# Kernel optimization log

Hardware: AMD Instinct MI355X
Metric: run time of the kernel (lower is better)

Reference implementation:

```python
import jax, jax.numpy as jnp
import numpy as np

H = 2048
V = 32000
N = 2048  # batch*seq tokens
IGNORE_INDEX = -100
TEMPERATURE = 1.0
W_HARD = 0.5
W_SOFT = 0.5


def setup_inputs() -> dict:
    key = jax.random.key(0)
    k1, k2, k3, k4, k5 = jax.random.split(key, 5)
    student_input = jax.random.normal(k1, (N, H // 2), dtype=jnp.float32)
    teacher_input = jax.random.normal(k2, (N, H), dtype=jnp.float32)
    target = jax.random.randint(k3, (N,), 0, V, dtype=jnp.int64)
    # learned params: Linear(in, out=V, bias=False) -> weight shape (V, in)
    student_weight = jax.random.normal(k4, (V, H // 2), dtype=jnp.float32) * 0.02
    teacher_weight = jax.random.normal(k5, (V, H), dtype=jnp.float32) * 0.02
    return {
        "student_input": student_input,
        "teacher_input": teacher_input,
        "student_weight": student_weight,
        "teacher_weight": teacher_weight,
        "target": target,
    }


def reference(student_input, teacher_input, student_weight, teacher_weight, target):
    # Linear projections to vocab (teacher under no_grad in torch)
    student_logits = (student_input @ student_weight.T).astype(jnp.float32)  # (N, V)
    teacher_logits = jax.lax.stop_gradient(
        (teacher_input @ teacher_weight.T).astype(jnp.float32)
    )  # (N, V)

    # Hard loss: cross-entropy with ignore_index, mean over valid tokens
    log_probs = jax.nn.log_softmax(student_logits, axis=-1)
    valid = target != IGNORE_INDEX
    safe_tgt = jnp.where(valid, target, 0)
    nll = -jnp.take_along_axis(log_probs, safe_tgt[:, None], axis=-1)[:, 0]
    n_valid = jnp.maximum(valid.sum(), 1)
    hard_loss = jnp.sum(jnp.where(valid, nll, 0.0)) / n_valid

    # Soft loss: Jensen-Shannon divergence with batchmean reduction
    sl = student_logits / TEMPERATURE
    tl = teacher_logits / TEMPERATURE
    student_probs = jax.nn.softmax(sl, axis=-1)
    teacher_probs = jax.nn.softmax(tl, axis=-1)
    log_mean = jnp.log((student_probs + teacher_probs) * 0.5)
    log_sp = jnp.log(student_probs)
    log_tp = jnp.log(teacher_probs)
    n = sl.shape[0]
    # kl_div(log_mean, log_p, log_target=True, batchmean) = sum(p*(log_p - log_mean))/n
    student_kl = jnp.sum(student_probs * (log_sp - log_mean)) / n
    teacher_kl = jnp.sum(teacher_probs * (log_tp - log_mean)) / n
    jsd_loss = (student_kl + teacher_kl) * 0.5

    return W_HARD * hard_loss + W_SOFT * jsd_loss
```

## Files before the change

kernel.cpp:

```cpp
#include <hip/hip_runtime.h>

#define VOCAB 32000
#define NTOK 2048
#define IGNORE_INDEX (-100)

typedef unsigned short u16;
typedef unsigned int u32;
typedef __bf16 bf16x8 __attribute__((ext_vector_type(8)));
typedef float floatx4 __attribute__((ext_vector_type(4)));

__device__ __forceinline__ u16 f2bf(float f) {
    u32 u = __float_as_uint(f);
    u32 r = u + 0x7fffu + ((u >> 16) & 1u);
    return (u16)(r >> 16);
}
__device__ __forceinline__ float bf2f(u32 lo16) {
    return __uint_as_float(lo16 << 16);
}

__global__ __launch_bounds__(256) void cvt_kernel(const float* __restrict__ in,
                                                  u16* __restrict__ out, int n4) {
    int i = blockIdx.x * 256 + threadIdx.x;
    if (i >= n4) return;
    float4 v = ((const float4*)in)[i];
    ushort4 o;
    o.x = f2bf(v.x); o.y = f2bf(v.y); o.z = f2bf(v.z); o.w = f2bf(v.w);
    ((ushort4*)out)[i] = o;
}

__global__ __launch_bounds__(256) void gemm_bt_kernel(
    const u16* __restrict__ A, const u16* __restrict__ B, u16* __restrict__ C,
    int M, int N, int K)
{
    __shared__ u16 lds_a[128 * 64];
    __shared__ u16 lds_b[128 * 64];

    const int tid  = threadIdx.x;
    const int lane = tid & 63;
    const int wave = tid >> 6;
    const int bm = blockIdx.x * 128;
    const int bn = blockIdx.y * 128;
    const int wm = (wave >> 1) * 64;
    const int wn = (wave & 1) * 64;

    floatx4 acc[4][4] = {};

    const int l8 = lane >> 3;
    const int c8 = lane & 7;
    const int srow = wave * 8 + l8;
    const int scol = ((c8 ^ l8) << 3);
    const u16* agp = A + (size_t)(bm + srow) * K + scol;
    const u16* bgp = B + (size_t)(bn + srow) * K + scol;

    for (int k0 = 0; k0 < K; k0 += 64) {
#pragma unroll
        for (int c = 0; c < 4; ++c) {
            __builtin_amdgcn_global_load_lds(
                (const __attribute__((address_space(1))) u32*)(agp + k0 + (size_t)c * 32 * K),
                (__attribute__((address_space(3))) u32*)(lds_a + wave * 512 + c * 2048),
                16, 0, 0);
            __builtin_amdgcn_global_load_lds(
                (const __attribute__((address_space(1))) u32*)(bgp + k0 + (size_t)c * 32 * K),
                (__attribute__((address_space(3))) u32*)(lds_b + wave * 512 + c * 2048),
                16, 0, 0);
        }
        __syncthreads();
#pragma unroll
        for (int s = 0; s < 2; ++s) {
            const int swz = (((s * 4) + (lane >> 4)) ^ (lane & 7)) << 3;
            bf16x8 af[4], bq[4];
#pragma unroll
            for (int i = 0; i < 4; ++i)
                af[i] = *(const bf16x8*)(lds_a + (wm + i * 16 + (lane & 15)) * 64 + swz);
#pragma unroll
            for (int j = 0; j < 4; ++j)
                bq[j] = *(const bf16x8*)(lds_b + (wn + j * 16 + (lane & 15)) * 64 + swz);
#pragma unroll
            for (int i = 0; i < 4; ++i)
#pragma unroll
                for (int j = 0; j < 4; ++j)
                    acc[i][j] = __builtin_amdgcn_mfma_f32_16x16x32_bf16(af[i], bq[j], acc[i][j], 0, 0, 0);
        }
        __syncthreads();
    }

#pragma unroll
    for (int i = 0; i < 4; ++i) {
        const int r0 = bm + wm + i * 16 + (lane >> 4) * 4;
#pragma unroll
        for (int j = 0; j < 4; ++j) {
            const int c0 = bn + wn + j * 16 + (lane & 15);
#pragma unroll
            for (int r = 0; r < 4; ++r)
                C[(size_t)(r0 + r) * N + c0] = f2bf(acc[i][j][r]);
        }
    }
}

__global__ __launch_bounds__(256) void rowstats_kernel(
    const u16* __restrict__ Ls, const u16* __restrict__ Lt,
    const int* __restrict__ tgt, float* __restrict__ rows)
{
    const int n    = blockIdx.x;
    const int tid  = threadIdx.x;
    const int lane = tid & 63;
    const int wave = tid >> 6;

    const u16* lsrow = Ls + (size_t)n * VOCAB;
    const u16* ltrow = Lt + (size_t)n * VOCAB;
    const uint4* ls4 = (const uint4*)lsrow;
    const uint4* lt4 = (const uint4*)ltrow;
    const int V8 = VOCAB / 8;

    float ss = 0.f, st = 0.f;
    for (int v = tid; v < V8; v += 256) {
        uint4 a = ls4[v], b = lt4[v];
        ss += __expf(bf2f(a.x & 0xffffu)) + __expf(bf2f(a.x >> 16))
            + __expf(bf2f(a.y & 0xffffu)) + __expf(bf2f(a.y >> 16))
            + __expf(bf2f(a.z & 0xffffu)) + __expf(bf2f(a.z >> 16))
            + __expf(bf2f(a.w & 0xffffu)) + __expf(bf2f(a.w >> 16));
        st += __expf(bf2f(b.x & 0xffffu)) + __expf(bf2f(b.x >> 16))
            + __expf(bf2f(b.y & 0xffffu)) + __expf(bf2f(b.y >> 16))
            + __expf(bf2f(b.z & 0xffffu)) + __expf(bf2f(b.z >> 16))
            + __expf(bf2f(b.w & 0xffffu)) + __expf(bf2f(b.w >> 16));
    }
#pragma unroll
    for (int off = 32; off > 0; off >>= 1) {
        ss += __shfl_down(ss, off);
        st += __shfl_down(st, off);
    }
    __shared__ float shm[4][2];
    __shared__ float lse_sh[2];
    if (lane == 0) { shm[wave][0] = ss; shm[wave][1] = st; }
    __syncthreads();
    if (tid == 0) {
        float s0 = shm[0][0] + shm[1][0] + shm[2][0] + shm[3][0];
        float s1 = shm[0][1] + shm[1][1] + shm[2][1] + shm[3][1];
        lse_sh[0] = logf(s0);
        lse_sh[1] = logf(s1);
    }
    __syncthreads();
    const float lse_s = lse_sh[0];
    const float lse_t = lse_sh[1];

    float jacc = 0.f;
    for (int v = tid; v < V8; v += 256) {
        uint4 a = ls4[v], b = lt4[v];
        u32 pa[4] = {a.x, a.y, a.z, a.w};
        u32 pb[4] = {b.x, b.y, b.z, b.w};
#pragma unroll
        for (int q = 0; q < 4; ++q) {
            float lsp0 = bf2f(pa[q] & 0xffffu) - lse_s, lsp1 = bf2f(pa[q] >> 16) - lse_s;
            float ltp0 = bf2f(pb[q] & 0xffffu) - lse_t, ltp1 = bf2f(pb[q] >> 16) - lse_t;
            float sp0 = __expf(lsp0), sp1 = __expf(lsp1);
            float tp0 = __expf(ltp0), tp1 = __expf(ltp1);
            float lm0 = logf(0.5f * (sp0 + tp0));
            float lm1 = logf(0.5f * (sp1 + tp1));
            jacc += sp0 * (lsp0 - lm0) + tp0 * (ltp0 - lm0);
            jacc += sp1 * (lsp1 - lm1) + tp1 * (ltp1 - lm1);
        }
    }
#pragma unroll
    for (int off = 32; off > 0; off >>= 1) jacc += __shfl_down(jacc, off);
    __shared__ float jsh[4];
    if (lane == 0) jsh[wave] = jacc;
    __syncthreads();
    if (tid == 0) {
        float j = jsh[0] + jsh[1] + jsh[2] + jsh[3];
        int t = tgt[n];
        bool valid = (t != IGNORE_INDEX);
        float nll = 0.f;
        if (valid) nll = lse_s - bf2f((u32)lsrow[t]);
        rows[n * 3 + 0] = nll;
        rows[n * 3 + 1] = valid ? 1.f : 0.f;
        rows[n * 3 + 2] = j;
    }
}

__global__ __launch_bounds__(256) void final_kernel(const float* __restrict__ rows,
                                                    float* __restrict__ out) {
    const int tid = threadIdx.x;
    float a = 0.f, b = 0.f, c = 0.f;
    for (int i = tid; i < NTOK; i += 256) {
        a += rows[i * 3]; b += rows[i * 3 + 1]; c += rows[i * 3 + 2];
    }
#pragma unroll
    for (int off = 32; off > 0; off >>= 1) {
        a += __shfl_down(a, off);
        b += __shfl_down(b, off);
        c += __shfl_down(c, off);
    }
    __shared__ float sh[4][3];
    const int lane = tid & 63, wave = tid >> 6;
    if (lane == 0) { sh[wave][0] = a; sh[wave][1] = b; sh[wave][2] = c; }
    __syncthreads();
    if (tid == 0) {
        a = sh[0][0] + sh[1][0] + sh[2][0] + sh[3][0];
        b = sh[0][1] + sh[1][1] + sh[2][1] + sh[3][1];
        c = sh[0][2] + sh[1][2] + sh[2][2] + sh[3][2];
        float nv = fmaxf(b, 1.f);
        out[0] = 0.5f * (a / nv) + 0.25f * (c / (float)NTOK);
    }
}

extern "C" void kernel_launch(void* const* d_in, const int* in_sizes, int n_in,
                              void* d_out, int out_size, void* d_ws, size_t ws_size,
                              hipStream_t stream)
{
    const float* s_in = (const float*)d_in[0];
    const float* t_in = (const float*)d_in[1];
    const float* s_w  = (const float*)d_in[2];
    const float* t_w  = (const float*)d_in[3];
    const int*   tgt  = (const int*)d_in[4];

    u16* sA = (u16*)d_ws;
    u16* tA = sA + (size_t)NTOK * 1024;
    u16* sW = tA + (size_t)NTOK * 2048;
    u16* tW = sW + (size_t)VOCAB * 1024;
    u16* Ls = tW + (size_t)VOCAB * 2048;
    u16* Lt = Ls + (size_t)NTOK * VOCAB;
    float* rows = (float*)(Lt + (size_t)NTOK * VOCAB);

    int n4;
    n4 = NTOK * 1024 / 4;  cvt_kernel<<<(n4 + 255) / 256, 256, 0, stream>>>(s_in, sA, n4);
    n4 = NTOK * 2048 / 4;  cvt_kernel<<<(n4 + 255) / 256, 256, 0, stream>>>(t_in, tA, n4);
    n4 = VOCAB * 1024 / 4; cvt_kernel<<<(n4 + 255) / 256, 256, 0, stream>>>(s_w, sW, n4);
    n4 = VOCAB * 2048 / 4; cvt_kernel<<<(n4 + 255) / 256, 256, 0, stream>>>(t_w, tW, n4);

    dim3 g(NTOK / 128, VOCAB / 128);
    gemm_bt_kernel<<<g, 256, 0, stream>>>(sA, sW, Ls, NTOK, VOCAB, 1024);
    gemm_bt_kernel<<<g, 256, 0, stream>>>(tA, tW, Lt, NTOK, VOCAB, 2048);

    rowstats_kernel<<<NTOK, 256, 0, stream>>>(Ls, Lt, tgt, rows);
    final_kernel<<<1, 256, 0, stream>>>(rows, (float*)d_out);
}
```

Measured before the change: 1.040 ms.

## Fuse row exp-sum into GEMM epilogue via LDS-staged coalesced stores

The GEMM epilogue now stages the bf16 output tile in LDS with a swizzle, writes it back with coalesced 16-byte stores, and computes per-row partial sums of exp(logit) that are atomically added into a global rowsum buffer. The rowstats kernel drops its first pass over both logit matrices and reads the log-sum-exp from rowsum, removing one full read of the logits. The GEMM loop also uses incremented pointers, and fast __logf replaces logf. This costs an extra zero kernel, atomics contention (250 column blocks per row), and nondeterministic summation order.

Result: no change. 1.030 ms (-0.9%).

```diff
diff --git a/kernel.cpp b/kernel.cpp
--- a/kernel.cpp
+++ b/kernel.cpp
@@ -28,12 +28,18 @@
     ((ushort4*)out)[i] = o;
 }
 
+__global__ __launch_bounds__(256) void zero_kernel(float* __restrict__ p, int n) {
+    int i = blockIdx.x * 256 + threadIdx.x;
+    if (i < n) p[i] = 0.f;
+}
+
 __global__ __launch_bounds__(256) void gemm_bt_kernel(
     const u16* __restrict__ A, const u16* __restrict__ B, u16* __restrict__ C,
-    int M, int N, int K)
+    float* __restrict__ rowsum, int M, int N, int K)
 {
-    __shared__ u16 lds_a[128 * 64];
-    __shared__ u16 lds_b[128 * 64];
+    __shared__ u16 lds[2 * 128 * 64];
+    u16* lds_a = lds;
+    u16* lds_b = lds + 128 * 64;
 
     const int tid  = threadIdx.x;
     const int lane = tid & 63;
@@ -49,21 +55,34 @@
     const int c8 = lane & 7;
     const int srow = wave * 8 + l8;
     const int scol = ((c8 ^ l8) << 3);
-    const u16* agp = A + (size_t)(bm + srow) * K + scol;
-    const u16* bgp = B + (size_t)(bn + srow) * K + scol;
+    const u16* ap0 = A + (size_t)(bm + srow) * K + scol;
+    const u16* ap1 = ap0 + (size_t)32 * K;
+    const u16* ap2 = ap0 + (size_t)64 * K;
+    const u16* ap3 = ap0 + (size_t)96 * K;
+    const u16* bp0 = B + (size_t)(bn + srow) * K + scol;
+    const u16* bp1 = bp0 + (size_t)32 * K;
+    const u16* bp2 = bp0 + (size_t)64 * K;
+    const u16* bp3 = bp0 + (size_t)96 * K;
 
     for (int k0 = 0; k0 < K; k0 += 64) {
-#pragma unroll
-        for (int c = 0; c < 4; ++c) {
-            __builtin_amdgcn_global_load_lds(
-                (const __attribute__((address_space(1))) u32*)(agp + k0 + (size_t)c * 32 * K),
-                (__attribute__((address_space(3))) u32*)(lds_a + wave * 512 + c * 2048),
-                16, 0, 0);
-            __builtin_amdgcn_global_load_lds(
-                (const __attribute__((address_space(1))) u32*)(bgp + k0 + (size_t)c * 32 * K),
-                (__attribute__((address_space(3))) u32*)(lds_b + wave * 512 + c * 2048),
-                16, 0, 0);
-        }
+        __builtin_amdgcn_global_load_lds((const __attribute__((address_space(1))) u32*)ap0,
+            (__attribute__((address_space(3))) u32*)(lds_a + wave * 512 + 0 * 2048), 16, 0, 0);
+        __builtin_amdgcn_global_load_lds((const __attribute__((address_space(1))) u32*)ap1,
+            (__attribute__((address_space(3))) u32*)(lds_a + wave * 512 + 1 * 2048), 16, 0, 0);
+        __builtin_amdgcn_global_load_lds((const __attribute__((address_space(1))) u32*)ap2,
+            (__attribute__((address_space(3))) u32*)(lds_a + wave * 512 + 2 * 2048), 16, 0, 0);
+        __builtin_amdgcn_global_load_lds((const __attribute__((address_space(1))) u32*)ap3,
+            (__attribute__((address_space(3))) u32*)(lds_a + wave * 512 + 3 * 2048), 16, 0, 0);
+        __builtin_amdgcn_global_load_lds((const __attribute__((address_space(1))) u32*)bp0,
+            (__attribute__((address_space(3))) u32*)(lds_b + wave * 512 + 0 * 2048), 16, 0, 0);
+        __builtin_amdgcn_global_load_lds((const __attribute__((address_space(1))) u32*)bp1,
+            (__attribute__((address_space(3))) u32*)(lds_b + wave * 512 + 1 * 2048), 16, 0, 0);
+        __builtin_amdgcn_global_load_lds((const __attribute__((address_space(1))) u32*)bp2,
+            (__attribute__((address_space(3))) u32*)(lds_b + wave * 512 + 2 * 2048), 16, 0, 0);
+        __builtin_amdgcn_global_load_lds((const __attribute__((address_space(1))) u32*)bp3,
+            (__attribute__((address_space(3))) u32*)(lds_b + wave * 512 + 3 * 2048), 16, 0, 0);
+        ap0 += 64; ap1 += 64; ap2 += 64; ap3 += 64;
+        bp0 += 64; bp1 += 64; bp2 += 64; bp3 += 64;
         __syncthreads();
 #pragma unroll
         for (int s = 0; s < 2; ++s) {
@@ -84,22 +103,46 @@
         __syncthreads();
     }
 
+    const int q = lane >> 4;
+    const int cl = lane & 15;
 #pragma unroll
     for (int i = 0; i < 4; ++i) {
-        const int r0 = bm + wm + i * 16 + (lane >> 4) * 4;
 #pragma unroll
         for (int j = 0; j < 4; ++j) {
-            const int c0 = bn + wn + j * 16 + (lane & 15);
-#pragma unroll
-            for (int r = 0; r < 4; ++r)
-                C[(size_t)(r0 + r) * N + c0] = f2bf(acc[i][j][r]);
+            const int col = wn + j * 16 + cl;
+#pragma unroll
+            for (int r = 0; r < 4; ++r) {
+                const int row = wm + i * 16 + q * 4 + r;
+                lds[row * 128 + ((((col >> 3) ^ (row & 15)) << 3) | (col & 7))] =
+                    f2bf(acc[i][j][r]);
+            }
         }
+    }
+    __syncthreads();
+
+#pragma unroll
+    for (int p = 0; p < 8; ++p) {
+        const int idx = p * 256 + tid;
+        const int row = idx >> 4;
+        const int ch  = idx & 15;
+        uint4 v = *(const uint4*)(lds + row * 128 + ((ch ^ (row & 15)) << 3));
+        *(uint4*)(C + (size_t)(bm + row) * N + bn + ch * 8) = v;
+        float se = __expf(bf2f(v.x & 0xffffu)) + __expf(bf2f(v.x >> 16))
+                 + __expf(bf2f(v.y & 0xffffu)) + __expf(bf2f(v.y >> 16))
+                 + __expf(bf2f(v.z & 0xffffu)) + __expf(bf2f(v.z >> 16))
+                 + __expf(bf2f(v.w & 0xffffu)) + __expf(bf2f(v.w >> 16));
+        se += __shfl_xor(se, 1);
+        se += __shfl_xor(se, 2);
+        se += __shfl_xor(se, 4);
+        se += __shfl_xor(se, 8);
+        if ((tid & 15) == 0) atomicAdd(rowsum + bm + row, se);
     }
 }
 
 __global__ __launch_bounds__(256) void rowstats_kernel(
     const u16* __restrict__ Ls, const u16* __restrict__ Lt,
-    const int* __restrict__ tgt, float* __restrict__ rows)
+    const float* __restrict__ rowsum, const int* __restrict__ tgt,
+    float* __restrict__ rows)
 {
     const int n    = blockIdx.x;
     const int tid  = threadIdx.x;
@@ -112,36 +155,8 @@
     const uint4* lt4 = (const uint4*)ltrow;
     const int V8 = VOCAB / 8;
 
-    float ss = 0.f, st = 0.f;
-    for (int v = tid; v < V8; v += 256) {
-        uint4 a = ls4[v], b = lt4[v];
-        ss += __expf(bf2f(a.x & 0xffffu)) + __expf(bf2f(a.x >> 16))
-            + __expf(bf2f(a.y & 0xffffu)) + __expf(bf2f(a.y >> 16))
-            + __expf(bf2f(a.z & 0xffffu)) + __expf(bf2f(a.z >> 16))
-            + __expf(bf2f(a.w & 0xffffu)) + __expf(bf2f(a.w >> 16));
-        st += __expf(bf2f(b.x & 0xffffu)) + __expf(bf2f(b.x >> 16))
-            + __expf(bf2f(b.y & 0xffffu)) + __expf(bf2f(b.y >> 16))
-            + __expf(bf2f(b.z & 0xffffu)) + __expf(bf2f(b.z >> 16))
-            + __expf(bf2f(b.w & 0xffffu)) + __expf(bf2f(b.w >> 16));
-    }
-#pragma unroll
-    for (int off = 32; off > 0; off >>= 1) {
-        ss += __shfl_down(ss, off);
-        st += __shfl_down(st, off);
-    }
-    __shared__ float shm[4][2];
-    __shared__ float lse_sh[2];
-    if (lane == 0) { shm[wave][0] = ss; shm[wave][1] = st; }
-    __syncthreads();
-    if (tid == 0) {
-        float s0 = shm[0][0] + shm[1][0] + shm[2][0] + shm[3][0];
-        float s1 = shm[0][1] + shm[1][1] + shm[2][1] + shm[3][1];
-        lse_sh[0] = logf(s0);
-        lse_sh[1] = logf(s1);
-    }
-    __syncthreads();
-    const float lse_s = lse_sh[0];
-    const float lse_t = lse_sh[1];
+    const float lse_s = __logf(rowsum[n]);
+    const float lse_t = __logf(rowsum[NTOK + n]);
 
     float jacc = 0.f;
     for (int v = tid; v < V8; v += 256) {
@@ -149,13 +164,13 @@
         u32 pa[4] = {a.x, a.y, a.z, a.w};
         u32 pb[4] = {b.x, b.y, b.z, b.w};
 #pragma unroll
-        for (int q = 0; q < 4; ++q) {
-            float lsp0 = bf2f(pa[q] & 0xffffu) - lse_s, lsp1 = bf2f(pa[q] >> 16) - lse_s;
-            float ltp0 = bf2f(pb[q] & 0xffffu) - lse_t, ltp1 = bf2f(pb[q] >> 16) - lse_t;
+        for (int qq = 0; qq < 4; ++qq) {
+            float lsp0 = bf2f(pa[qq] & 0xffffu) - lse_s, lsp1 = bf2f(pa[qq] >> 16) - lse_s;
+            float ltp0 = bf2f(pb[qq] & 0xffffu) - lse_t, ltp1 = bf2f(pb[qq] >> 16) - lse_t;
             float sp0 = __expf(lsp0), sp1 = __expf(lsp1);
             float tp0 = __expf(ltp0), tp1 = __expf(ltp1);
-            float lm0 = logf(0.5f * (sp0 + tp0));
-            float lm1 = logf(0.5f * (sp1 + tp1));
+            float lm0 = __logf(0.5f * (sp0 + tp0));
+            float lm1 = __logf(0.5f * (sp1 + tp1));
             jacc += sp0 * (lsp0 - lm0) + tp0 * (ltp0 - lm0);
             jacc += sp1 * (lsp1 - lm1) + tp1 * (ltp1 - lm1);
         }
@@ -219,18 +234,20 @@
     u16* tW = sW + (size_t)VOCAB * 1024;
     u16* Ls = tW + (size_t)VOCAB * 2048;
     u16* Lt = Ls + (size_t)NTOK * VOCAB;
-    float* rows = (float*)(Lt + (size_t)NTOK * VOCAB);
+    float* rows   = (float*)(Lt + (size_t)NTOK * VOCAB);
+    float* rowsum = rows + NTOK * 3;
 
     int n4;
     n4 = NTOK * 1024 / 4;  cvt_kernel<<<(n4 + 255) / 256, 256, 0, stream>>>(s_in, sA, n4);
     n4 = NTOK * 2048 / 4;  cvt_kernel<<<(n4 + 255) / 256, 256, 0, stream>>>(t_in, tA, n4);
     n4 = VOCAB * 1024 / 4; cvt_kernel<<<(n4 + 255) / 256, 256, 0, stream>>>(s_w, sW, n4);
     n4 = VOCAB * 2048 / 4; cvt_kernel<<<(n4 + 255) / 256, 256, 0, stream>>>(t_w, tW, n4);
+    zero_kernel<<<(2 * NTOK + 255) / 256, 256, 0, stream>>>(rowsum, 2 * NTOK);
 
     dim3 g(NTOK / 128, VOCAB / 128);
-    gemm_bt_kernel<<<g, 256, 0, stream>>>(sA, sW, Ls, NTOK, VOCAB, 1024);
-    gemm_bt_kernel<<<g, 256, 0, stream>>>(tA, tW, Lt, NTOK, VOCAB, 2048);
-
-    rowstats_kernel<<<NTOK, 256, 0, stream>>>(Ls, Lt, tgt, rows);
+    gemm_bt_kernel<<<g, 256, 0, stream>>>(sA, sW, Ls, rowsum,        NTOK, VOCAB, 1024);
+    gemm_bt_kernel<<<g, 256, 0, stream>>>(tA, tW, Lt, rowsum + NTOK, NTOK, VOCAB, 2048);
+
+    rowstats_kernel<<<NTOK, 256, 0, stream>>>(Ls, Lt, rowsum, tgt, rows);
     final_kernel<<<1, 256, 0, stream>>>(rows, (float*)d_out);
 }
```
